# Performance work log

Hardware: AMD Instinct MI355X
Metric: run time of the kernel (lower is better)

Reference implementation:

```python
import jax, jax.numpy as jnp
import numpy as np

DIM = 1024
HEADS = 16
DIM_HEAD = 64
INNER = HEADS * DIM_HEAD
SEQ = 4096
BATCH = 1


def setup_inputs() -> dict:
    key = jax.random.key(0)
    ks = jax.random.split(key, 6)
    s = 0.02
    return {
        "x": jax.random.normal(ks[0], (BATCH, SEQ, DIM), dtype=jnp.float32),
        "Wq": jax.random.normal(ks[1], (DIM, INNER), dtype=jnp.float32) * s,
        "Wk": jax.random.normal(ks[2], (DIM, INNER), dtype=jnp.float32) * s,
        "Wv": jax.random.normal(ks[3], (DIM, INNER), dtype=jnp.float32) * s,
        "Wo": jax.random.normal(ks[4], (INNER, DIM), dtype=jnp.float32) * s,
        "bo": jax.random.normal(ks[5], (DIM,), dtype=jnp.float32) * s,
    }


def reference(x, Wq, Wk, Wv, Wo, bo):
    b, n, _ = x.shape
    beta = 1.0 / jnp.sqrt(jnp.float32(DIM_HEAD))
    # project and split heads: [b, n, inner] -> [b, h, n, d]
    def split_heads(t):
        return t.reshape(b, n, HEADS, DIM_HEAD).transpose(0, 2, 1, 3)
    q = split_heads(x @ Wq)
    k = split_heads(x @ Wk)
    v = split_heads(x @ Wv)
    # scaled scores [b, h, n, n]
    scores = jnp.einsum('bhid,bhjd->bhij', q * beta, k)
    mask_value = -jnp.finfo(scores.dtype).max
    causal = jnp.triu(jnp.ones((n, n), dtype=bool), k=1)
    scores = jnp.where(causal, mask_value, scores)
    attn = jax.nn.softmax(scores, axis=-1)
    out = jnp.einsum('bhij,bhjd->bhid', attn, v)
    out = out.transpose(0, 2, 1, 3).reshape(b, n, INNER)
    # output projection (dropout is identity in eval)
    return out @ Wo + bo
```

## Files before the change

### kernel.cpp

```cpp
#include <hip/hip_runtime.h>
#include <hip/hip_bf16.h>
#include <stdint.h>

#define SEQ 4096
#define DIM 1024
#define NHEADS 16
#define DHEAD 64
#define INNER 1024

typedef __hip_bfloat16 bf16;
typedef __attribute__((ext_vector_type(8))) short short8;
typedef __attribute__((ext_vector_type(4))) float floatx4;

__device__ __forceinline__ void gll16(const bf16* g, bf16* l) {
    __builtin_amdgcn_global_load_lds(
        (const __attribute__((address_space(1))) unsigned int*)g,
        (__attribute__((address_space(3))) unsigned int*)l,
        16, 0, 0);
}

__device__ __forceinline__ unsigned short f2bf_bits(float f) {
    bf16 h = __float2bfloat16(f);
    return *reinterpret_cast<unsigned short*>(&h);
}

__device__ __forceinline__ uint2 pack4bf(float a, float b, float c, float d) {
    uint2 r;
    r.x = (unsigned)f2bf_bits(a) | ((unsigned)f2bf_bits(b) << 16);
    r.y = (unsigned)f2bf_bits(c) | ((unsigned)f2bf_bits(d) << 16);
    return r;
}

__global__ __launch_bounds__(256) void convert_x_kernel(const float* __restrict__ x,
                                                        bf16* __restrict__ xb) {
    int i = (blockIdx.x * 256 + threadIdx.x) * 4;
    float4 f = *reinterpret_cast<const float4*>(x + i);
    unsigned long long p = (unsigned long long)f2bf_bits(f.x)
                         | ((unsigned long long)f2bf_bits(f.y) << 16)
                         | ((unsigned long long)f2bf_bits(f.z) << 32)
                         | ((unsigned long long)f2bf_bits(f.w) << 48);
    *reinterpret_cast<unsigned long long*>(xb + i) = p;
}

__global__ __launch_bounds__(256) void transpose_w_kernel(
        const float* __restrict__ W0, const float* __restrict__ W1,
        const float* __restrict__ W2, const float* __restrict__ W3,
        bf16* __restrict__ T0, bf16* __restrict__ T1,
        bf16* __restrict__ T2, bf16* __restrict__ T3) {
    const float* W; bf16* T;
    switch (blockIdx.z) {
        case 0:  W = W0; T = T0; break;
        case 1:  W = W1; T = T1; break;
        case 2:  W = W2; T = T2; break;
        default: W = W3; T = T3; break;
    }
    __shared__ float tile[32][33];
    int k0 = blockIdx.x * 32, n0 = blockIdx.y * 32;
    int tx = threadIdx.x, ty = threadIdx.y;
    #pragma unroll
    for (int i = 0; i < 4; i++)
        tile[ty + 8 * i][tx] = W[(size_t)(k0 + ty + 8 * i) * 1024 + n0 + tx];
    __syncthreads();
    #pragma unroll
    for (int i = 0; i < 4; i++)
        T[(size_t)(n0 + ty + 8 * i) * 1024 + k0 + tx] = __float2bfloat16(tile[tx][ty + 8 * i]);
}

__global__ __launch_bounds__(256) void transpose_v_kernel(const bf16* __restrict__ Vh,
                                                          bf16* __restrict__ Vt) {
    __shared__ bf16 tile[32][33];
    int h = blockIdx.z;
    int n0 = blockIdx.x * 32, d0 = blockIdx.y * 32;
    int tx = threadIdx.x, ty = threadIdx.y;
    const bf16* src = Vh + (size_t)h * SEQ * DHEAD;
    bf16* dst = Vt + (size_t)h * DHEAD * SEQ;
    #pragma unroll
    for (int i = 0; i < 4; i++)
        tile[ty + 8 * i][tx] = src[(size_t)(n0 + ty + 8 * i) * DHEAD + d0 + tx];
    __syncthreads();
    #pragma unroll
    for (int i = 0; i < 4; i++)
        dst[(size_t)(d0 + ty + 8 * i) * SEQ + n0 + tx] = tile[tx][ty + 8 * i];
}

__device__ __forceinline__ void gemm128_body(const bf16* __restrict__ A,
                                             const bf16* __restrict__ Bt,
                                             int m0, int n0, floatx4 acc[4][4]) {
    __shared__ __align__(16) bf16 As[8192];
    __shared__ __align__(16) bf16 Bs[8192];
    const int tid = threadIdx.x;
    const int wave = tid >> 6;
    const int lane = tid & 63;
    const int l15 = lane & 15;
    const int quad = lane >> 4;

    #pragma unroll
    for (int i = 0; i < 4; i++)
        #pragma unroll
        for (int j = 0; j < 4; j++)
            acc[i][j] = (floatx4){0.f, 0.f, 0.f, 0.f};

    for (int k0 = 0; k0 < 1024; k0 += 64) {
        __syncthreads();
        #pragma unroll
        for (int j = 0; j < 4; j++) {
            int t = wave * 4 + j;
            int row = (t >> 1) * 16 + l15;
            int kb = (t & 1) * 32 + quad * 8;
            gll16(A + (size_t)(m0 + row) * 1024 + k0 + kb, &As[t * 512]);
            gll16(Bt + (size_t)(n0 + row) * 1024 + k0 + kb, &Bs[t * 512]);
        }
        __syncthreads();
        #pragma unroll
        for (int ks = 0; ks < 2; ks++) {
            short8 af[4], bfr[4];
            #pragma unroll
            for (int i = 0; i < 4; i++)
                af[i] = *reinterpret_cast<const short8*>(
                    &As[((((wave >> 1) * 4 + i) * 2 + ks) * 512) + lane * 8]);
            #pragma unroll
            for (int j = 0; j < 4; j++)
                bfr[j] = *reinterpret_cast<const short8*>(
                    &Bs[((((wave & 1) * 4 + j) * 2 + ks) * 512) + lane * 8]);
            #pragma unroll
            for (int i = 0; i < 4; i++)
                #pragma unroll
                for (int j = 0; j < 4; j++)
                    acc[i][j] = __builtin_amdgcn_mfma_f32_16x16x32_bf16(af[i], bfr[j], acc[i][j], 0, 0, 0);
        }
    }
}

__global__ __launch_bounds__(256) void qkv_gemm_kernel(
        const bf16* __restrict__ xb,
        const bf16* __restrict__ Wqt, const bf16* __restrict__ Wkt, const bf16* __restrict__ Wvt,
        bf16* __restrict__ Qh, bf16* __restrict__ Kh, bf16* __restrict__ Vh) {
    const bf16* Bt; bf16* O; float scale = 1.0f;
    if (blockIdx.z == 0)      { Bt = Wqt; O = Qh; scale = 0.125f; }
    else if (blockIdx.z == 1) { Bt = Wkt; O = Kh; }
    else                      { Bt = Wvt; O = Vh; }
    int n0 = blockIdx.x * 128, m0 = blockIdx.y * 128;
    floatx4 acc[4][4];
    gemm128_body(xb, Bt, m0, n0, acc);

    const int tid = threadIdx.x, wave = tid >> 6, lane = tid & 63;
    const int l15 = lane & 15, quad = lane >> 4;
    const int wm = (wave >> 1) * 64, wn = (wave & 1) * 64;
    #pragma unroll
    for (int i = 0; i < 4; i++)
        #pragma unroll
        for (int j = 0; j < 4; j++) {
            int col = n0 + wn + j * 16 + l15;
            int h = col >> 6, d = col & 63;
            #pragma unroll
            for (int r = 0; r < 4; r++) {
                int row = m0 + wm + i * 16 + quad * 4 + r;
                O[((size_t)h * SEQ + row) * DHEAD + d] = __float2bfloat16(acc[i][j][r] * scale);
            }
        }
}

__global__ __launch_bounds__(256) void out_gemm_kernel(
        const bf16* __restrict__ Oa, const bf16* __restrict__ Wot,
        const float* __restrict__ bo, float* __restrict__ out) {
    int n0 = blockIdx.x * 128, m0 = blockIdx.y * 128;
    floatx4 acc[4][4];
    gemm128_body(Oa, Wot, m0, n0, acc);

    const int tid = threadIdx.x, wave = tid >> 6, lane = tid & 63;
    const int l15 = lane & 15, quad = lane >> 4;
    const int wm = (wave >> 1) * 64, wn = (wave & 1) * 64;
    #pragma unroll
    for (int i = 0; i < 4; i++)
        #pragma unroll
        for (int j = 0; j < 4; j++) {
            int col = n0 + wn + j * 16 + l15;
            float b = bo[col];
            #pragma unroll
            for (int r = 0; r < 4; r++) {
                int row = m0 + wm + i * 16 + quad * 4 + r;
                out[(size_t)row * DIM + col] = acc[i][j][r] + b;
            }
        }
}

__global__ __launch_bounds__(256, 4) void attention_kernel(
        const bf16* __restrict__ Qh, const bf16* __restrict__ Kh,
        const bf16* __restrict__ Vt, bf16* __restrict__ Oa) {
    __shared__ __align__(16) bf16 Ksh[8192];
    __shared__ __align__(16) bf16 Vsh[8192];
    __shared__ __align__(16) bf16 Ps[4][2048];
    const int tid = threadIdx.x, wave = tid >> 6, lane = tid & 63;
    const int l15 = lane & 15, quad = lane >> 4;
    const int id = blockIdx.x;
    const int head = id & 15;
    const int qt = 63 - (id >> 4);
    const int qw = qt * 64 + wave * 16;
    const size_t hoff = (size_t)head * SEQ * DHEAD;
    const bf16* Qb = Qh + hoff;
    const bf16* Kb = Kh + hoff;
    const bf16* Vb = Vt + hoff;

    short8 bq[2];
    #pragma unroll
    for (int s = 0; s < 2; s++)
        bq[s] = *reinterpret_cast<const short8*>(Qb + (size_t)(qw + l15) * DHEAD + s * 32 + quad * 8);

    floatx4 acc_o[4];
    #pragma unroll
    for (int c = 0; c < 4; c++) acc_o[c] = (floatx4){0.f, 0.f, 0.f, 0.f};
    float l_part = 0.f;

    const int ntiles = (qt + 2) >> 1;
    for (int kt = 0; kt < ntiles; kt++) {
        const int kbase = kt * 128;
        __syncthreads();
        #pragma unroll
        for (int j = 0; j < 4; j++) {
            int t = wave * 4 + j;
            gll16(Kb + (size_t)(kbase + (t >> 1) * 16 + l15) * DHEAD + (t & 1) * 32 + quad * 8,
                  &Ksh[t * 512]);
            gll16(Vb + (size_t)((t >> 2) * 16 + l15) * SEQ + kbase + (t & 3) * 32 + quad * 8,
                  &Vsh[t * 512]);
        }
        __syncthreads();

        floatx4 st[8];
        #pragma unroll
        for (int c = 0; c < 8; c++) st[c] = (floatx4){0.f, 0.f, 0.f, 0.f};
        #pragma unroll
        for (int c = 0; c < 8; c++) {
            short8 ak0 = *reinterpret_cast<const short8*>(&Ksh[(c * 2 + 0) * 512 + lane * 8]);
            short8 ak1 = *reinterpret_cast<const short8*>(&Ksh[(c * 2 + 1) * 512 + lane * 8]);
            st[c] = __builtin_amdgcn_mfma_f32_16x16x32_bf16(ak0, bq[0], st[c], 0, 0, 0);
            st[c] = __builtin_amdgcn_mfma_f32_16x16x32_bf16(ak1, bq[1], st[c], 0, 0, 0);
        }
        if (kbase + 127 > qw) {
            int base0 = kbase + quad * 4 - qw - l15;
            #pragma unroll
            for (int c = 0; c < 8; c++) {
                int base = base0 + c * 16;
                #pragma unroll
                for (int r = 0; r < 4; r++)
                    if (base + r > 0) st[c][r] = -1e30f;
            }
        }
        #pragma unroll
        for (int c = 0; c < 8; c++) {
            float p0 = __expf(st[c][0]);
            float p1 = __expf(st[c][1]);
            float p2 = __expf(st[c][2]);
            float p3 = __expf(st[c][3]);
            l_part += (p0 + p1) + (p2 + p3);
            int elem = (c >> 1) * 512 + (l15 + 16 * ((c & 1) * 2 + (quad >> 1))) * 8 + (quad & 1) * 4;
            *reinterpret_cast<uint2*>(&Ps[wave][elem]) = pack4bf(p0, p1, p2, p3);
        }
        #pragma unroll
        for (int s = 0; s < 4; s++) {
            short8 bp = *reinterpret_cast<const short8*>(&Ps[wave][s * 512 + lane * 8]);
            #pragma unroll
            for (int c = 0; c < 4; c++) {
                short8 av = *reinterpret_cast<const short8*>(&Vsh[(c * 4 + s) * 512 + lane * 8]);
                acc_o[c] = __builtin_amdgcn_mfma_f32_16x16x32_bf16(av, bp, acc_o[c], 0, 0, 0);
            }
        }
    }
    float l = l_part;
    l += __shfl_xor(l, 16, 64);
    l += __shfl_xor(l, 32, 64);
    float rcp = 1.0f / l;
    const int q = qw + l15;
    #pragma unroll
    for (int c = 0; c < 4; c++) {
        uint2 v = pack4bf(acc_o[c][0] * rcp, acc_o[c][1] * rcp,
                          acc_o[c][2] * rcp, acc_o[c][3] * rcp);
        *reinterpret_cast<uint2*>(Oa + (size_t)q * INNER + head * DHEAD + c * 16 + quad * 4) = v;
    }
}

extern "C" void kernel_launch(void* const* d_in, const int* in_sizes, int n_in,
                              void* d_out, int out_size, void* d_ws, size_t ws_size,
                              hipStream_t stream) {
    const float* x  = (const float*)d_in[0];
    const float* Wq = (const float*)d_in[1];
    const float* Wk = (const float*)d_in[2];
    const float* Wv = (const float*)d_in[3];
    const float* Wo = (const float*)d_in[4];
    const float* bo = (const float*)d_in[5];
    float* out = (float*)d_out;

    char* ws = (char*)d_ws;
    size_t off = 0;
    bf16* xb  = (bf16*)(ws + off); off += (size_t)SEQ * DIM * 2;
    bf16* Wqt = (bf16*)(ws + off); off += (size_t)DIM * INNER * 2;
    bf16* Wkt = (bf16*)(ws + off); off += (size_t)DIM * INNER * 2;
    bf16* Wvt = (bf16*)(ws + off); off += (size_t)DIM * INNER * 2;
    bf16* Wot = (bf16*)(ws + off); off += (size_t)INNER * DIM * 2;
    bf16* Qh  = (bf16*)(ws + off); off += (size_t)NHEADS * SEQ * DHEAD * 2;
    bf16* Kh  = (bf16*)(ws + off); off += (size_t)NHEADS * SEQ * DHEAD * 2;
    bf16* Vh  = (bf16*)(ws + off); off += (size_t)NHEADS * SEQ * DHEAD * 2;
    bf16* Vtr = (bf16*)(ws + off); off += (size_t)NHEADS * DHEAD * SEQ * 2;
    bf16* Oa  = (bf16*)(ws + off); off += (size_t)SEQ * INNER * 2;

    convert_x_kernel<<<(SEQ * DIM) / 1024, 256, 0, stream>>>(x, xb);
    transpose_w_kernel<<<dim3(32, 32, 4), dim3(32, 8), 0, stream>>>(Wq, Wk, Wv, Wo,
                                                                    Wqt, Wkt, Wvt, Wot);
    qkv_gemm_kernel<<<dim3(8, 32, 3), 256, 0, stream>>>(xb, Wqt, Wkt, Wvt, Qh, Kh, Vh);
    transpose_v_kernel<<<dim3(SEQ / 32, DHEAD / 32, NHEADS), dim3(32, 8), 0, stream>>>(Vh, Vtr);
    attention_kernel<<<1024, 256, 0, stream>>>(Qh, Kh, Vtr, Oa);
    out_gemm_kernel<<<dim3(8, 32), 256, 0, stream>>>(Oa, Wot, bo, out);
}
```

Before: 257.8 us.

## Fuse V transpose into QKV GEMM, load V fragments directly, reorder attention tiles

The QKV GEMM epilogue now writes V straight into the transposed per-head layout as packed 4-element stores, which removes the separate transpose kernel and the intermediate V buffer. Attention loads V fragments from global memory into registers, split into two halves so the loads overlap with the QK MMAs, and drops the V shared-memory tile. log2(e) is folded into the Q scale so softmax can use exp2f. Query tiles are assigned in a serpentine order instead of longest-first, and bf16 packing uses the paired conversion intrinsic. The costs are higher register pressure and global V reads issued by every wave instead of shared staging, and the new tile order may balance causal work worse.

```diff
diff --git a/kernel.cpp b/kernel.cpp
--- a/kernel.cpp
+++ b/kernel.cpp
@@ -1,6 +1,7 @@
 #include <hip/hip_runtime.h>
 #include <hip/hip_bf16.h>
 #include <stdint.h>
+#include <math.h>
 
 #define SEQ 4096
 #define DIM 1024
@@ -25,9 +26,11 @@
 }
 
 __device__ __forceinline__ uint2 pack4bf(float a, float b, float c, float d) {
+    __hip_bfloat162 lo = __float22bfloat162_rn(float2{a, b});
+    __hip_bfloat162 hi = __float22bfloat162_rn(float2{c, d});
     uint2 r;
-    r.x = (unsigned)f2bf_bits(a) | ((unsigned)f2bf_bits(b) << 16);
-    r.y = (unsigned)f2bf_bits(c) | ((unsigned)f2bf_bits(d) << 16);
+    r.x = *reinterpret_cast<unsigned*>(&lo);
+    r.y = *reinterpret_cast<unsigned*>(&hi);
     return r;
 }
 
@@ -66,23 +69,6 @@
         T[(size_t)(n0 + ty + 8 * i) * 1024 + k0 + tx] = __float2bfloat16(tile[tx][ty + 8 * i]);
 }
 
-__global__ __launch_bounds__(256) void transpose_v_kernel(const bf16* __restrict__ Vh,
-                                                          bf16* __restrict__ Vt) {
-    __shared__ bf16 tile[32][33];
-    int h = blockIdx.z;
-    int n0 = blockIdx.x * 32, d0 = blockIdx.y * 32;
-    int tx = threadIdx.x, ty = threadIdx.y;
-    const bf16* src = Vh + (size_t)h * SEQ * DHEAD;
-    bf16* dst = Vt + (size_t)h * DHEAD * SEQ;
-    #pragma unroll
-    for (int i = 0; i < 4; i++)
-        tile[ty + 8 * i][tx] = src[(size_t)(n0 + ty + 8 * i) * DHEAD + d0 + tx];
-    __syncthreads();
-    #pragma unroll
-    for (int i = 0; i < 4; i++)
-        dst[(size_t)(d0 + ty + 8 * i) * SEQ + n0 + tx] = tile[tx][ty + 8 * i];
-}
-
 __device__ __forceinline__ void gemm128_body(const bf16* __restrict__ A,
                                              const bf16* __restrict__ Bt,
                                              int m0, int n0, floatx4 acc[4][4]) {
@@ -134,11 +120,11 @@
 __global__ __launch_bounds__(256) void qkv_gemm_kernel(
         const bf16* __restrict__ xb,
         const bf16* __restrict__ Wqt, const bf16* __restrict__ Wkt, const bf16* __restrict__ Wvt,
-        bf16* __restrict__ Qh, bf16* __restrict__ Kh, bf16* __restrict__ Vh) {
-    const bf16* Bt; bf16* O; float scale = 1.0f;
-    if (blockIdx.z == 0)      { Bt = Wqt; O = Qh; scale = 0.125f; }
-    else if (blockIdx.z == 1) { Bt = Wkt; O = Kh; }
-    else                      { Bt = Wvt; O = Vh; }
+        bf16* __restrict__ Qh, bf16* __restrict__ Kh, bf16* __restrict__ Vt) {
+    const bf16* Bt;
+    if (blockIdx.z == 0)      Bt = Wqt;
+    else if (blockIdx.z == 1) Bt = Wkt;
+    else                      Bt = Wvt;
     int n0 = blockIdx.x * 128, m0 = blockIdx.y * 128;
     floatx4 acc[4][4];
     gemm128_body(xb, Bt, m0, n0, acc);
@@ -146,18 +132,33 @@
     const int tid = threadIdx.x, wave = tid >> 6, lane = tid & 63;
     const int l15 = lane & 15, quad = lane >> 4;
     const int wm = (wave >> 1) * 64, wn = (wave & 1) * 64;
-    #pragma unroll
-    for (int i = 0; i < 4; i++)
-        #pragma unroll
-        for (int j = 0; j < 4; j++) {
-            int col = n0 + wn + j * 16 + l15;
-            int h = col >> 6, d = col & 63;
-            #pragma unroll
-            for (int r = 0; r < 4; r++) {
-                int row = m0 + wm + i * 16 + quad * 4 + r;
-                O[((size_t)h * SEQ + row) * DHEAD + d] = __float2bfloat16(acc[i][j][r] * scale);
+    if (blockIdx.z == 2) {
+        #pragma unroll
+        for (int i = 0; i < 4; i++)
+            #pragma unroll
+            for (int j = 0; j < 4; j++) {
+                int col = n0 + wn + j * 16 + l15;
+                int h = col >> 6, d = col & 63;
+                int row0 = m0 + wm + i * 16 + quad * 4;
+                uint2 v = pack4bf(acc[i][j][0], acc[i][j][1], acc[i][j][2], acc[i][j][3]);
+                *reinterpret_cast<uint2*>(Vt + ((size_t)h * DHEAD + d) * SEQ + row0) = v;
             }
-        }
+    } else {
+        bf16* O = (blockIdx.z == 0) ? Qh : Kh;
+        float scale = (blockIdx.z == 0) ? 0.125f * 1.4426950408889634f : 1.0f;
+        #pragma unroll
+        for (int i = 0; i < 4; i++)
+            #pragma unroll
+            for (int j = 0; j < 4; j++) {
+                int col = n0 + wn + j * 16 + l15;
+                int h = col >> 6, d = col & 63;
+                #pragma unroll
+                for (int r = 0; r < 4; r++) {
+                    int row = m0 + wm + i * 16 + quad * 4 + r;
+                    O[((size_t)h * SEQ + row) * DHEAD + d] = __float2bfloat16(acc[i][j][r] * scale);
+                }
+            }
+    }
 }
 
 __global__ __launch_bounds__(256) void out_gemm_kernel(
@@ -188,13 +189,14 @@
         const bf16* __restrict__ Qh, const bf16* __restrict__ Kh,
         const bf16* __restrict__ Vt, bf16* __restrict__ Oa) {
     __shared__ __align__(16) bf16 Ksh[8192];
-    __shared__ __align__(16) bf16 Vsh[8192];
     __shared__ __align__(16) bf16 Ps[4][2048];
     const int tid = threadIdx.x, wave = tid >> 6, lane = tid & 63;
     const int l15 = lane & 15, quad = lane >> 4;
     const int id = blockIdx.x;
     const int head = id & 15;
-    const int qt = 63 - (id >> 4);
+    const int rid = id >> 4;
+    const int low = rid & 15, hi = rid >> 4;
+    const int qt = hi * 16 + ((hi & 1) ? (15 - low) : low);
     const int qw = qt * 64 + wave * 16;
     const size_t hoff = (size_t)head * SEQ * DHEAD;
     const bf16* Qb = Qh + hoff;
@@ -204,12 +206,15 @@
     short8 bq[2];
     #pragma unroll
     for (int s = 0; s < 2; s++)
-        bq[s] = *reinterpret_cast<const short8*>(Qb + (size_t)(qw + l15) * DHEAD + s * 32 + quad * 8);
+        bq[s] = *reinterpret_cast<const short8*>(
+            Qb + (size_t)(qw + l15) * DHEAD + s * 32 + quad * 8);
 
     floatx4 acc_o[4];
     #pragma unroll
     for (int c = 0; c < 4; c++) acc_o[c] = (floatx4){0.f, 0.f, 0.f, 0.f};
     float l_part = 0.f;
+
+    const bf16* vp0 = Vb + (size_t)l15 * SEQ + quad * 8;
 
     const int ntiles = (qt + 2) >> 1;
     for (int kt = 0; kt < ntiles; kt++) {
@@ -220,9 +225,14 @@
             int t = wave * 4 + j;
             gll16(Kb + (size_t)(kbase + (t >> 1) * 16 + l15) * DHEAD + (t & 1) * 32 + quad * 8,
                   &Ksh[t * 512]);
-            gll16(Vb + (size_t)((t >> 2) * 16 + l15) * SEQ + kbase + (t & 3) * 32 + quad * 8,
-                  &Vsh[t * 512]);
-        }
+        }
+        short8 av0[2][4];
+        #pragma unroll
+        for (int s = 0; s < 2; s++)
+            #pragma unroll
+            for (int c = 0; c < 4; c++)
+                av0[s][c] = *reinterpret_cast<const short8*>(
+                    vp0 + (size_t)(c * 16) * SEQ + kbase + s * 32);
         __syncthreads();
 
         floatx4 st[8];
@@ -235,6 +245,13 @@
             st[c] = __builtin_amdgcn_mfma_f32_16x16x32_bf16(ak0, bq[0], st[c], 0, 0, 0);
             st[c] = __builtin_amdgcn_mfma_f32_16x16x32_bf16(ak1, bq[1], st[c], 0, 0, 0);
         }
+        short8 av1[2][4];
+        #pragma unroll
+        for (int s = 0; s < 2; s++)
+            #pragma unroll
+            for (int c = 0; c < 4; c++)
+                av1[s][c] = *reinterpret_cast<const short8*>(
+                    vp0 + (size_t)(c * 16) * SEQ + kbase + (s + 2) * 32);
         if (kbase + 127 > qw) {
             int base0 = kbase + quad * 4 - qw - l15;
             #pragma unroll
@@ -247,22 +264,28 @@
         }
         #pragma unroll
         for (int c = 0; c < 8; c++) {
-            float p0 = __expf(st[c][0]);
-            float p1 = __expf(st[c][1]);
-            float p2 = __expf(st[c][2]);
-            float p3 = __expf(st[c][3]);
+            float p0 = exp2f(st[c][0]);
+            float p1 = exp2f(st[c][1]);
+            float p2 = exp2f(st[c][2]);
+            float p3 = exp2f(st[c][3]);
             l_part += (p0 + p1) + (p2 + p3);
-            int elem = (c >> 1) * 512 + (l15 + 16 * ((c & 1) * 2 + (quad >> 1))) * 8 + (quad & 1) * 4;
+            int elem = (c >> 1) * 512
+                     + (l15 + 16 * ((c & 1) * 2 + (quad >> 1))) * 8 + (quad & 1) * 4;
             *reinterpret_cast<uint2*>(&Ps[wave][elem]) = pack4bf(p0, p1, p2, p3);
         }
         #pragma unroll
-        for (int s = 0; s < 4; s++) {
+        for (int s = 0; s < 2; s++) {
             short8 bp = *reinterpret_cast<const short8*>(&Ps[wave][s * 512 + lane * 8]);
             #pragma unroll
-            for (int c = 0; c < 4; c++) {
-                short8 av = *reinterpret_cast<const short8*>(&Vsh[(c * 4 + s) * 512 + lane * 8]);
-                acc_o[c] = __builtin_amdgcn_mfma_f32_16x16x32_bf16(av, bp, acc_o[c], 0, 0, 0);
-            }
+            for (int c = 0; c < 4; c++)
+                acc_o[c] = __builtin_amdgcn_mfma_f32_16x16x32_bf16(av0[s][c], bp, acc_o[c], 0, 0, 0);
+        }
+        #pragma unroll
+        for (int s = 0; s < 2; s++) {
+            short8 bp = *reinterpret_cast<const short8*>(&Ps[wave][(s + 2) * 512 + lane * 8]);
+            #pragma unroll
+            for (int c = 0; c < 4; c++)
+                acc_o[c] = __builtin_amdgcn_mfma_f32_16x16x32_bf16(av1[s][c], bp, acc_o[c], 0, 0, 0);
         }
     }
     float l = l_part;
@@ -298,15 +321,13 @@
     bf16* Wot = (bf16*)(ws + off); off += (size_t)INNER * DIM * 2;
     bf16* Qh  = (bf16*)(ws + off); off += (size_t)NHEADS * SEQ * DHEAD * 2;
     bf16* Kh  = (bf16*)(ws + off); off += (size_t)NHEADS * SEQ * DHEAD * 2;
-    bf16* Vh  = (bf16*)(ws + off); off += (size_t)NHEADS * SEQ * DHEAD * 2;
     bf16* Vtr = (bf16*)(ws + off); off += (size_t)NHEADS * DHEAD * SEQ * 2;
     bf16* Oa  = (bf16*)(ws + off); off += (size_t)SEQ * INNER * 2;
 
     convert_x_kernel<<<(SEQ * DIM) / 1024, 256, 0, stream>>>(x, xb);
     transpose_w_kernel<<<dim3(32, 32, 4), dim3(32, 8), 0, stream>>>(Wq, Wk, Wv, Wo,
                                                                     Wqt, Wkt, Wvt, Wot);
-    qkv_gemm_kernel<<<dim3(8, 32, 3), 256, 0, stream>>>(xb, Wqt, Wkt, Wvt, Qh, Kh, Vh);
-    transpose_v_kernel<<<dim3(SEQ / 32, DHEAD / 32, NHEADS), dim3(32, 8), 0, stream>>>(Vh, Vtr);
+    qkv_gemm_kernel<<<dim3(8, 32, 3), 256, 0, stream>>>(xb, Wqt, Wkt, Wvt, Qh, Kh, Vtr);
     attention_kernel<<<1024, 256, 0, stream>>>(Qh, Kh, Vtr, Oa);
     out_gemm_kernel<<<dim3(8, 32), 256, 0, stream>>>(Oa, Wot, bo, out);
 }
```

New measurement: 391.6 us. 51.9% more time.
